# Kernel optimization log

Hardware: AMD Instinct MI355X
Metric: run time of the kernel (lower is better)

The kernel has to match this reference:

```python
import jax, jax.numpy as jnp
import numpy as np
from jax import lax

SUBBANDS = 4
TAPS = 64
BETA = 9.0


def _qmf_filter():
    # scipy.signal.kaiser(M, beta) == np.kaiser(M, beta)
    h = np.kaiser(TAPS + 1, BETA)
    h = h / np.sum(h)
    n = np.arange(TAPS + 1)
    filt = [h * np.cos((2 * k + 1) * np.pi * n / (2 * SUBBANDS) + (-1) ** k * np.pi / 4)
            for k in range(SUBBANDS)]
    return np.asarray(filt, dtype=np.float32)  # [S, TAPS+1]


def setup_inputs() -> dict:
    key = jax.random.key(0)
    x = jax.random.normal(key, (16, 1, 524288), dtype=jnp.float32)
    qmf = jnp.asarray(_qmf_filter())
    return {"x": x, "qmf": qmf}


def reference(x, qmf):
    S = SUBBANDS
    pad = TAPS // 2  # 32
    # --- analysis: full conv then ::S decimation == strided conv (identical outputs) ---
    wa = qmf[:, None, :]  # [S, 1, TAPS+1] (OIW)
    sub = lax.conv_general_dilated(
        x, wa, window_strides=(S,), padding=[(pad, pad)],
        dimension_numbers=("NCH", "OIH", "NCH"))  # [B, S, T//S]
    # --- synthesis: zero-stuff upsample by S then conv, summed over subbands.
    # lhs_dilation=S inserts the zeros; right pad extra S-1 to match the
    # explicit x_up buffer (3 trailing zeros after the last sample).
    # Summing the S per-subband convs == one conv with S input channels.
    ws = qmf[None, :, :]  # [1, S, TAPS+1]
    y = lax.conv_general_dilated(
        sub, ws, window_strides=(1,), padding=[(pad, pad + S - 1)],
        lhs_dilation=(S,), dimension_numbers=("NCH", "OIH", "NCH"))  # [B, 1, T]
    return y
```

## Files before the change

### kernel.cpp

```cpp
#include <hip/hip_runtime.h>
#include <math.h>

#define NTAP 65
#define LEN 524288
#define LSUB 131072
#define BATCH 16
#define UT 1024
#define NSUB 1040
#define NXG 1056

struct Filt2 { float f0[NTAP]; float f1[NTAP]; };

__device__ __forceinline__ int swz(int g) { return g ^ ((g >> 3) & 7); }

__device__ __forceinline__ void analyze4(const float4* __restrict__ xs, int s0, int u0,
                                         const Filt2& F, float4* __restrict__ subs) {
    float w[80];
    #pragma unroll
    for (int j = 0; j < 20; j++) {
        float4 v = xs[swz(s0 + j)];
        w[4*j+0] = v.x; w[4*j+1] = v.y; w[4*j+2] = v.z; w[4*j+3] = v.w;
    }
    #pragma unroll
    for (int c = 0; c < 4; c++) {
        float e0 = 0.f, o0 = 0.f, e1 = 0.f, o1 = 0.f;
        #pragma unroll
        for (int n = 0; n < NTAP; n++) {
            float v = w[4*c + n];
            if (n & 1) { o0 = fmaf(F.f0[n], v, o0); o1 = fmaf(F.f1[n], v, o1); }
            else       { e0 = fmaf(F.f0[n], v, e0); e1 = fmaf(F.f1[n], v, e1); }
        }
        int i = u0 - 8 + s0 + c;
        float4 r = make_float4(e0 + o0, e1 + o1, e1 - o1, e0 - o0);
        if (i < 0 || i >= LSUB) r = make_float4(0.f, 0.f, 0.f, 0.f);
        subs[swz(s0 + c)] = r;
    }
}

__global__ __launch_bounds__(256, 4) void pqmf_fused(const float* __restrict__ x,
                                                     float* __restrict__ y, Filt2 F) {
    __shared__ float4 xs[NXG];
    __shared__ float4 subs[NSUB];

    const int t = threadIdx.x;
    const int b = blockIdx.x >> 7;
    const int u0 = (blockIdx.x & 127) << 10;
    const float* xb = x + (size_t)b * LEN;
    const int gbase = u0 - 16;

    if (gbase >= 0 && gbase + NXG <= LEN / 4) {
        #pragma unroll
        for (int p = 0; p < 4; p++)
            xs[swz(t + 256 * p)] = *reinterpret_cast<const float4*>(xb + 4 * (gbase + t + 256 * p));
        if (t < NXG - 1024)
            xs[swz(t + 1024)] = *reinterpret_cast<const float4*>(xb + 4 * (gbase + t + 1024));
    } else {
        for (int r = t; r < NXG; r += 256) {
            int g = gbase + r;
            float v[4];
            #pragma unroll
            for (int c2 = 0; c2 < 4; c2++) {
                int p = 4 * g + c2;
                v[c2] = (p >= 0 && p < LEN) ? xb[p] : 0.f;
            }
            xs[swz(r)] = make_float4(v[0], v[1], v[2], v[3]);
        }
    }
    __syncthreads();

    analyze4(xs, 4 * t, u0, F, subs);
    if ((t & 63) == 0) analyze4(xs, UT + 4 * (t >> 6), u0, F, subs);
    __syncthreads();

    float P[20], M[20], Q[20], R[20];
    #pragma unroll
    for (int j = 0; j < 20; j++) {
        float4 v = subs[swz(4 * t + j)];
        P[j] = v.x + v.w; M[j] = v.x - v.w;
        Q[j] = v.y + v.z; R[j] = v.y - v.z;
    }
    float* yb = y + (size_t)b * LEN;
    #pragma unroll
    for (int c = 0; c < 4; c++) {
        float a0 = 0.f, a1 = 0.f, a2 = 0.f, a3 = 0.f;
        #pragma unroll
        for (int j2 = 0; j2 <= 16; j2++) {
            a0 = fmaf(F.f0[4 * j2], P[c + j2], a0);
            a0 = fmaf(F.f1[4 * j2], Q[c + j2], a0);
        }
        #pragma unroll
        for (int j2 = 1; j2 <= 16; j2++) {
            a1 = fmaf(F.f0[4 * j2 - 1], M[c + j2], a1);
            a1 = fmaf(F.f1[4 * j2 - 1], R[c + j2], a1);
            a2 = fmaf(F.f0[4 * j2 - 2], P[c + j2], a2);
            a2 = fmaf(F.f1[4 * j2 - 2], Q[c + j2], a2);
            a3 = fmaf(F.f0[4 * j2 - 3], M[c + j2], a3);
            a3 = fmaf(F.f1[4 * j2 - 3], R[c + j2], a3);
        }
        *reinterpret_cast<float4*>(yb + 4 * (size_t)(u0 + 4 * t + c)) =
            make_float4(a0, a1, a2, a3);
    }
}

static double bessel_i0(double x) {
    double t = 1.0, s = 1.0;
    for (int m = 1; m < 80; m++) {
        double u = x / (2.0 * m);
        t *= u * u;
        s += t;
        if (t < s * 1e-18) break;
    }
    return s;
}

extern "C" void kernel_launch(void* const* d_in, const int* in_sizes, int n_in,
                              void* d_out, int out_size, void* d_ws, size_t ws_size,
                              hipStream_t stream) {
    const float* x = (const float*)d_in[0];
    float* y = (float*)d_out;

    Filt2 F;
    {
        double h[NTAP], sum = 0.0;
        double ib = bessel_i0(9.0);
        for (int n = 0; n < NTAP; n++) {
            double r = (n - 32.0) / 32.0;
            double arg = 1.0 - r * r;
            if (arg < 0.0) arg = 0.0;
            h[n] = bessel_i0(9.0 * sqrt(arg)) / ib;
            sum += h[n];
        }
        for (int n = 0; n < NTAP; n++) h[n] /= sum;
        const double PI = 3.14159265358979323846;
        for (int n = 0; n < NTAP; n++) {
            F.f0[n] = (float)(h[n] * cos(1.0 * PI * n / 8.0 + PI / 4.0));
            F.f1[n] = (float)(h[n] * cos(3.0 * PI * n / 8.0 - PI / 4.0));
        }
    }

    dim3 blk(256);
    dim3 grd(BATCH * (LSUB / UT));
    pqmf_fused<<<grd, blk, 0, stream>>>(x, y, F);
}
```

Measured before the change: 105.9 us.

## Collapse analysis+synthesis into one polyphase composite filter with edge corrections

```diff
diff --git a/kernel.cpp b/kernel.cpp
--- a/kernel.cpp
+++ b/kernel.cpp
@@ -1,116 +1,209 @@
 #include <hip/hip_runtime.h>
-#include <math.h>
-
-#define NTAP 65
+
 #define LEN 524288
 #define LSUB 131072
 #define BATCH 16
-#define UT 1024
-#define NSUB 1040
 #define NXG 1056
-
-struct Filt2 { float f0[NTAP]; float f1[NTAP]; };
+#define NTILE 128
+
+constexpr double csqrt_d(double a) {
+    double x = (a > 1.0) ? a : 1.0;
+    for (int i = 0; i < 64; i++) x = 0.5 * (x + a / x);
+    return x;
+}
+constexpr double i0_d(double x) {
+    double t = 1.0, s = 1.0;
+    for (int m = 1; m < 50; m++) { double u = x / (2.0 * m); t *= u * u; s += t; }
+    return s;
+}
+struct Tbl {
+    float f[4][65];
+    float C[4][129];
+};
+constexpr Tbl make_tbl() {
+    Tbl T{};
+    double h[65] = {};
+    double sum = 0.0;
+    const double ib = i0_d(9.0);
+    for (int n = 0; n < 65; n++) {
+        double r = (n - 32.0) / 32.0;
+        double a = 1.0 - r * r; if (a < 0) a = 0;
+        h[n] = i0_d(9.0 * csqrt_d(a)) / ib;
+        sum += h[n];
+    }
+    for (int n = 0; n < 65; n++) h[n] /= sum;
+    const double S2 = csqrt_d(2.0);
+    const double c1 = 0.5 * csqrt_d(2.0 + S2);
+    const double c2 = 0.5 * S2;
+    const double c3 = 0.5 * csqrt_d(2.0 - S2);
+    const double ct[16] = {1,c1,c2,c3,0,-c3,-c2,-c1,-1,-c1,-c2,-c3,0,c3,c2,c1};
+    double f[4][65] = {};
+    for (int k = 0; k < 4; k++)
+        for (int n = 0; n < 65; n++) {
+            int m = ((2 * k + 1) * n + ((k & 1) ? 14 : 2)) & 15;
+            f[k][n] = h[n] * ct[m];
+            T.f[k][n] = (float)f[k][n];
+        }
+    for (int p = 0; p < 4; p++)
+        for (int dd = -64; dd <= 64; dd++) {
+            double a = 0.0;
+            for (int k = 0; k < 4; k++)
+                for (int j = -8; j <= 8; j++) {
+                    int ia = 4 * j + 32 - p, ib2 = dd - 4 * j + 32;
+                    if (ia >= 0 && ia <= 64 && ib2 >= 0 && ib2 <= 64)
+                        a += f[k][ia] * f[k][ib2];
+                }
+            T.C[p][dd + 64] = (float)a;
+        }
+    return T;
+}
+static constexpr Tbl TBL = make_tbl();
 
 __device__ __forceinline__ int swz(int g) { return g ^ ((g >> 3) & 7); }
-
-__device__ __forceinline__ void analyze4(const float4* __restrict__ xs, int s0, int u0,
-                                         const Filt2& F, float4* __restrict__ subs) {
-    float w[80];
-    #pragma unroll
-    for (int j = 0; j < 20; j++) {
-        float4 v = xs[swz(s0 + j)];
-        w[4*j+0] = v.x; w[4*j+1] = v.y; w[4*j+2] = v.z; w[4*j+3] = v.w;
-    }
-    #pragma unroll
-    for (int c = 0; c < 4; c++) {
-        float e0 = 0.f, o0 = 0.f, e1 = 0.f, o1 = 0.f;
-        #pragma unroll
-        for (int n = 0; n < NTAP; n++) {
-            float v = w[4*c + n];
-            if (n & 1) { o0 = fmaf(F.f0[n], v, o0); o1 = fmaf(F.f1[n], v, o1); }
-            else       { e0 = fmaf(F.f0[n], v, e0); e1 = fmaf(F.f1[n], v, e1); }
-        }
-        int i = u0 - 8 + s0 + c;
-        float4 r = make_float4(e0 + o0, e1 + o1, e1 - o1, e0 - o0);
-        if (i < 0 || i >= LSUB) r = make_float4(0.f, 0.f, 0.f, 0.f);
-        subs[swz(s0 + c)] = r;
-    }
-}
-
-__global__ __launch_bounds__(256, 4) void pqmf_fused(const float* __restrict__ x,
-                                                     float* __restrict__ y, Filt2 F) {
+__device__ __forceinline__ float getc(const float4& v, int c) {
+    switch (c) { case 0: return v.x; case 1: return v.y; case 2: return v.z; default: return v.w; }
+}
+__device__ __forceinline__ float cpv(int p, int dlt) {
+    return (dlt < -64 || dlt > 64) ? 0.0f : TBL.C[p][dlt + 64];
+}
+__device__ __forceinline__ float lds_x(const float4* xs, int xi, int gbase) {
+    int r = (xi >> 2) - gbase;
+    return reinterpret_cast<const float*>(&xs[swz(r)])[xi & 3];
+}
+
+template <int TT>
+__device__ __forceinline__ void left_fix(const float4* xs, float (&acc)[4][4]) {
+    float sig[4][8];
+    #pragma unroll
+    for (int mi = 0; mi < 8; mi++) {
+        const int m = mi - 8;
+        float s0 = 0.f, s1 = 0.f, s2 = 0.f, s3 = 0.f;
+        #pragma unroll
+        for (int n = 32 - 4 * m; n <= 64; n++) {
+            float xv = lds_x(xs, 4 * m - 32 + n, -16);
+            s0 = fmaf(TBL.f[0][n], xv, s0);
+            s1 = fmaf(TBL.f[1][n], xv, s1);
+            s2 = fmaf(TBL.f[2][n], xv, s2);
+            s3 = fmaf(TBL.f[3][n], xv, s3);
+        }
+        sig[0][mi] = s0; sig[1][mi] = s1; sig[2][mi] = s2; sig[3][mi] = s3;
+    }
+    #pragma unroll
+    for (int o = 0; o < 4; o++) {
+        const int u = 4 * TT + o;
+        #pragma unroll
+        for (int p = 0; p < 4; p++) {
+            float s = 0.f;
+            #pragma unroll
+            for (int mi = 0; mi < 8; mi++) {
+                const int np = 4 * ((mi - 8) - u) + 32 - p;
+                if (np >= 0 && np <= 64) {
+                    s = fmaf(TBL.f[0][np], sig[0][mi], s);
+                    s = fmaf(TBL.f[1][np], sig[1][mi], s);
+                    s = fmaf(TBL.f[2][np], sig[2][mi], s);
+                    s = fmaf(TBL.f[3][np], sig[3][mi], s);
+                }
+            }
+            acc[o][p] -= s;
+        }
+    }
+}
+
+template <int TT>
+__device__ __forceinline__ void right_fix(const float4* xs, float (&acc)[4][4]) {
+    constexpr int GB = LSUB - 1040;
+    float sig[4][8];
+    #pragma unroll
+    for (int mi = 0; mi < 8; mi++) {
+        float s0 = 0.f, s1 = 0.f, s2 = 0.f, s3 = 0.f;
+        #pragma unroll
+        for (int n = 0; n <= 31 - 4 * mi; n++) {
+            float xv = lds_x(xs, 4 * (LSUB + mi) - 32 + n, GB);
+            s0 = fmaf(TBL.f[0][n], xv, s0);
+            s1 = fmaf(TBL.f[1][n], xv, s1);
+            s2 = fmaf(TBL.f[2][n], xv, s2);
+            s3 = fmaf(TBL.f[3][n], xv, s3);
+        }
+        sig[0][mi] = s0; sig[1][mi] = s1; sig[2][mi] = s2; sig[3][mi] = s3;
+    }
+    #pragma unroll
+    for (int o = 0; o < 4; o++) {
+        const int u = (LSUB - 1024) + 4 * TT + o;
+        #pragma unroll
+        for (int p = 0; p < 4; p++) {
+            float s = 0.f;
+            #pragma unroll
+            for (int mi = 0; mi < 8; mi++) {
+                const int np = 4 * ((LSUB + mi) - u) + 32 - p;
+                if (np >= 0 && np <= 64) {
+                    s = fmaf(TBL.f[0][np], sig[0][mi], s);
+                    s = fmaf(TBL.f[1][np], sig[1][mi], s);
+                    s = fmaf(TBL.f[2][np], sig[2][mi], s);
+                    s = fmaf(TBL.f[3][np], sig[3][mi], s);
+                }
+            }
+            acc[o][p] -= s;
+        }
+    }
+}
+
+__global__ __launch_bounds__(256, 8) void pqmf_composite(const float* __restrict__ x,
+                                                         float* __restrict__ y) {
     __shared__ float4 xs[NXG];
-    __shared__ float4 subs[NSUB];
 
     const int t = threadIdx.x;
     const int b = blockIdx.x >> 7;
-    const int u0 = (blockIdx.x & 127) << 10;
+    const int tile = blockIdx.x & (NTILE - 1);
+    const int u0 = tile << 10;
     const float* xb = x + (size_t)b * LEN;
     const int gbase = u0 - 16;
 
-    if (gbase >= 0 && gbase + NXG <= LEN / 4) {
-        #pragma unroll
-        for (int p = 0; p < 4; p++)
-            xs[swz(t + 256 * p)] = *reinterpret_cast<const float4*>(xb + 4 * (gbase + t + 256 * p));
+    if (gbase >= 0 && gbase + NXG <= LSUB) {
+        #pragma unroll
+        for (int q = 0; q < 4; q++)
+            xs[swz(t + 256 * q)] = *reinterpret_cast<const float4*>(xb + 4 * (gbase + t + 256 * q));
         if (t < NXG - 1024)
             xs[swz(t + 1024)] = *reinterpret_cast<const float4*>(xb + 4 * (gbase + t + 1024));
     } else {
         for (int r = t; r < NXG; r += 256) {
             int g = gbase + r;
-            float v[4];
+            float4 v = make_float4(0.f, 0.f, 0.f, 0.f);
+            if (g >= 0 && g < LSUB) v = *reinterpret_cast<const float4*>(xb + 4 * g);
+            xs[swz(r)] = v;
+        }
+    }
+    __syncthreads();
+
+    float acc[4][4] = {};
+    #pragma unroll
+    for (int d = -16; d <= 19; d++) {
+        float4 v = xs[swz(4 * t + 16 + d)];
+        #pragma unroll
+        for (int o = 0; o < 4; o++) {
+            const int e = d - o;
+            if (e < -16 || e > 16) continue;
             #pragma unroll
-            for (int c2 = 0; c2 < 4; c2++) {
-                int p = 4 * g + c2;
-                v[c2] = (p >= 0 && p < LEN) ? xb[p] : 0.f;
+            for (int p = 0; p < 4; p++) {
+                const int c0 = p & 1, c1 = (p & 1) + 2;
+                const float w0 = cpv(p, 4 * e + c0);
+                const float w1 = cpv(p, 4 * e + c1);
+                if (w0 != 0.f) acc[o][p] = fmaf(w0, getc(v, c0), acc[o][p]);
+                if (w1 != 0.f) acc[o][p] = fmaf(w1, getc(v, c1), acc[o][p]);
             }
-            xs[swz(r)] = make_float4(v[0], v[1], v[2], v[3]);
-        }
-    }
-    __syncthreads();
-
-    analyze4(xs, 4 * t, u0, F, subs);
-    if ((t & 63) == 0) analyze4(xs, UT + 4 * (t >> 6), u0, F, subs);
-    __syncthreads();
-
-    float P[20], M[20], Q[20], R[20];
-    #pragma unroll
-    for (int j = 0; j < 20; j++) {
-        float4 v = subs[swz(4 * t + j)];
-        P[j] = v.x + v.w; M[j] = v.x - v.w;
-        Q[j] = v.y + v.z; R[j] = v.y - v.z;
-    }
-    float* yb = y + (size_t)b * LEN;
-    #pragma unroll
-    for (int c = 0; c < 4; c++) {
-        float a0 = 0.f, a1 = 0.f, a2 = 0.f, a3 = 0.f;
-        #pragma unroll
-        for (int j2 = 0; j2 <= 16; j2++) {
-            a0 = fmaf(F.f0[4 * j2], P[c + j2], a0);
-            a0 = fmaf(F.f1[4 * j2], Q[c + j2], a0);
-        }
-        #pragma unroll
-        for (int j2 = 1; j2 <= 16; j2++) {
-            a1 = fmaf(F.f0[4 * j2 - 1], M[c + j2], a1);
-            a1 = fmaf(F.f1[4 * j2 - 1], R[c + j2], a1);
-            a2 = fmaf(F.f0[4 * j2 - 2], P[c + j2], a2);
-            a2 = fmaf(F.f1[4 * j2 - 2], Q[c + j2], a2);
-            a3 = fmaf(F.f0[4 * j2 - 3], M[c + j2], a3);
-            a3 = fmaf(F.f1[4 * j2 - 3], R[c + j2], a3);
-        }
-        *reinterpret_cast<float4*>(yb + 4 * (size_t)(u0 + 4 * t + c)) =
-            make_float4(a0, a1, a2, a3);
-    }
-}
-
-static double bessel_i0(double x) {
-    double t = 1.0, s = 1.0;
-    for (int m = 1; m < 80; m++) {
-        double u = x / (2.0 * m);
-        t *= u * u;
-        s += t;
-        if (t < s * 1e-18) break;
-    }
-    return s;
+        }
+    }
+
+    if (tile == 0 && t < 2) {
+        if (t == 0) left_fix<0>(xs, acc); else left_fix<1>(xs, acc);
+    }
+    if (tile == NTILE - 1 && t >= 254) {
+        if (t == 254) right_fix<254>(xs, acc); else right_fix<255>(xs, acc);
+    }
+
+    float4* yb = reinterpret_cast<float4*>(y + (size_t)b * LEN);
+    #pragma unroll
+    for (int o = 0; o < 4; o++)
+        yb[u0 + 4 * t + o] = make_float4(acc[o][0], acc[o][1], acc[o][2], acc[o][3]);
 }
 
 extern "C" void kernel_launch(void* const* d_in, const int* in_sizes, int n_in,
@@ -118,27 +211,7 @@
                               hipStream_t stream) {
     const float* x = (const float*)d_in[0];
     float* y = (float*)d_out;
-
-    Filt2 F;
-    {
-        double h[NTAP], sum = 0.0;
-        double ib = bessel_i0(9.0);
-        for (int n = 0; n < NTAP; n++) {
-            double r = (n - 32.0) / 32.0;
-            double arg = 1.0 - r * r;
-            if (arg < 0.0) arg = 0.0;
-            h[n] = bessel_i0(9.0 * sqrt(arg)) / ib;
-            sum += h[n];
-        }
-        for (int n = 0; n < NTAP; n++) h[n] /= sum;
-        const double PI = 3.14159265358979323846;
-        for (int n = 0; n < NTAP; n++) {
-            F.f0[n] = (float)(h[n] * cos(1.0 * PI * n / 8.0 + PI / 4.0));
-            F.f1[n] = (float)(h[n] * cos(3.0 * PI * n / 8.0 - PI / 4.0));
-        }
-    }
-
     dim3 blk(256);
-    dim3 grd(BATCH * (LSUB / UT));
-    pqmf_fused<<<grd, blk, 0, stream>>>(x, y, F);
-}
+    dim3 grd(BATCH * NTILE);
+    pqmf_composite<<<grd, blk, 0, stream>>>(x, y);
+}
```

Result: no change. 104.2 us (-1.6%).
